# Kernel optimization log

Hardware: AMD Instinct MI355X
Metric: run time of the kernel (lower is better)

## Reference

```python
import jax, jax.numpy as jnp
import numpy as np

# Model dims (match init_kwargs)
D_MODEL = 2048
H = 16        # query heads
HKV = 4       # kv heads (GQA)
DS = 32       # semantic head dim (compressed)
DG = 32       # geometric head dim (compressed, RoPE'd)
DV = 64       # value head dim
B, T = 2, 4096
MB = 64       # mem_block
LW = 1024     # local_window
ROPE_BASE = 10000.0
NEG_INF = -1e9


def _rope(x, pos, base):
    # x: [B, h, T, d] with d even; standard rotate-half RoPE
    d = x.shape[-1]
    inv_freq = 1.0 / (base ** (jnp.arange(0, d, 2, dtype=jnp.float32) / d))
    ang = pos.astype(jnp.float32)[:, None] * inv_freq          # [T, d/2]
    cos, sin = jnp.cos(ang), jnp.sin(ang)                      # [T, d/2]
    x1, x2 = jnp.split(x, 2, axis=-1)
    return jnp.concatenate([x1 * cos - x2 * sin,
                            x2 * cos + x1 * sin], axis=-1)


def setup_inputs() -> dict:
    key = jax.random.key(0)
    ks = jax.random.split(key, 8)
    w = lambda k, sh: jax.random.normal(k, sh, jnp.float32) * 0.02
    return {
        "x": jax.random.normal(ks[0], (B, T, D_MODEL), jnp.float32),
        "Wq_sem": w(ks[1], (D_MODEL, H * DS)),
        "Wk_sem": w(ks[2], (D_MODEL, HKV * DS)),
        "Wq_geo": w(ks[3], (D_MODEL, H * DG)),
        "Wk_geo": w(ks[4], (D_MODEL, HKV * DG)),
        "Wv": w(ks[5], (D_MODEL, HKV * DV)),
        "Wo": w(ks[6], (H * DV, D_MODEL)),
        "logit_scale": jnp.zeros((H,), jnp.float32),
    }


def reference(x, Wq_sem, Wk_sem, Wq_geo, Wk_geo, Wv, Wo, logit_scale):
    Bq, Tq = x.shape[0], x.shape[1]
    split = lambda y, h, d: y.reshape(Bq, Tq, h, d).transpose(0, 2, 1, 3)
    # Decoupled projections
    q_sem = split(x @ Wq_sem, H, DS)      # [B,H,T,DS]
    k_sem = split(x @ Wk_sem, HKV, DS)    # [B,HKV,T,DS]
    q_geo = split(x @ Wq_geo, H, DG)
    k_geo = split(x @ Wk_geo, HKV, DG)
    v = split(x @ Wv, HKV, DV)            # [B,HKV,T,DV]
    pos = jnp.arange(Tq)
    # RoPE only on the geometric path
    q_geo = _rope(q_geo, pos, ROPE_BASE)
    k_geo = _rope(k_geo, pos, ROPE_BASE)
    # Memory-block summarization: mean-pool remote KV into one token per block
    remote = Tq - LW
    nblk = remote // MB
    pool = lambda a: jnp.concatenate(
        [a[:, :, :remote].reshape(Bq, HKV, nblk, MB, a.shape[-1]).mean(axis=3),
         a[:, :, remote:]], axis=2)
    k_sem2, k_geo2, v2 = pool(k_sem), pool(k_geo), pool(v)  # [B,HKV,K,*], K=nblk+LW
    k_pos = jnp.concatenate([jnp.arange(nblk) * MB + (MB - 1),
                             jnp.arange(remote, Tq)])        # [K]
    # GQA head-group broadcast
    rep = lambda a: jnp.repeat(a, H // HKV, axis=1)
    k_sem2, k_geo2, v2 = rep(k_sem2), rep(k_geo2), rep(v2)   # [B,H,K,*]
    # Decoupled scores: semantic + geometric, each with its own scale
    scores = (jnp.einsum('bhqd,bhkd->bhqk', q_sem, k_sem2) * (1.0 / jnp.sqrt(float(DS)))
              + jnp.einsum('bhqd,bhkd->bhqk', q_geo, k_geo2) * (1.0 / jnp.sqrt(float(DG))))
    # Learned per-head temperature
    scores = scores * jnp.exp(logit_scale)[None, :, None, None]
    # Causal mask over summarized key positions
    mask = k_pos[None, :] <= pos[:, None]                    # [T,K]
    scores = jnp.where(mask[None, None], scores, NEG_INF)
    probs = jax.nn.softmax(scores, axis=-1)
    out = jnp.einsum('bhqk,bhkd->bhqd', probs, v2)           # [B,H,T,DV]
    out = out.transpose(0, 2, 1, 3).reshape(Bq, Tq, H * DV)
    return out @ Wo                                          # [B,T,D_MODEL]
```

## Files before the change

### kernel.cpp

```cpp
#include <hip/hip_runtime.h>
#include <math.h>

#define B_  2
#define T_  4096
#define DM  2048
#define H_  16
#define HKV 4
#define DV_ 64
#define MB_ 64
#define LW_ 1024
#define REMOTE 3072
#define NBLK 48
#define KTOT 1072
#define NTILES 17

typedef __bf16 bf16x8 __attribute__((ext_vector_type(8)));
typedef float  f32x4  __attribute__((ext_vector_type(4)));

__device__ __forceinline__ float bf2f(unsigned short u) {
    unsigned int x = ((unsigned int)u) << 16;
    return __builtin_bit_cast(float, x);
}
__device__ __forceinline__ unsigned short f2bf(float f) {
    unsigned int x = __builtin_bit_cast(unsigned int, f);
    x = x + 0x7fffu + ((x >> 16) & 1u);
    return (unsigned short)(x >> 16);
}

__device__ __forceinline__ void gload16(const void* gsrc, unsigned short* ldst) {
    __builtin_amdgcn_global_load_lds(
        (const __attribute__((address_space(1))) void*)gsrc,
        (__attribute__((address_space(3))) void*)ldst,
        16, 0, 0);
}

__global__ void transpose_all(const float* __restrict__ Wq_sem,
                              const float* __restrict__ Wq_geo,
                              const float* __restrict__ Wk_sem,
                              const float* __restrict__ Wk_geo,
                              const float* __restrict__ Wv,
                              const float* __restrict__ Wo,
                              unsigned short* __restrict__ WcatT,
                              unsigned short* __restrict__ WoT) {
    __shared__ float tile[32][33];
    const int bid = blockIdx.x;
    const float* src; unsigned short* dst; int R, C, tiles_x, lt;
    if (bid < 1024)      { src = Wq_sem; dst = WcatT;                       R = 2048; C = 512;  tiles_x = 16; lt = bid; }
    else if (bid < 2048) { src = Wq_geo; dst = WcatT + (size_t)512  * 2048; R = 2048; C = 512;  tiles_x = 16; lt = bid - 1024; }
    else if (bid < 2304) { src = Wk_sem; dst = WcatT + (size_t)1024 * 2048; R = 2048; C = 128;  tiles_x = 4;  lt = bid - 2048; }
    else if (bid < 2560) { src = Wk_geo; dst = WcatT + (size_t)1152 * 2048; R = 2048; C = 128;  tiles_x = 4;  lt = bid - 2304; }
    else if (bid < 3072) { src = Wv;     dst = WcatT + (size_t)1280 * 2048; R = 2048; C = 256;  tiles_x = 8;  lt = bid - 2560; }
    else                 { src = Wo;     dst = WoT;                         R = 1024; C = 2048; tiles_x = 64; lt = bid - 3072; }
    const int ct = lt % tiles_x, rt = lt / tiles_x;
    const int tx = threadIdx.x, ty = threadIdx.y;
    #pragma unroll
    for (int i = ty; i < 32; i += 8)
        tile[i][tx] = src[(size_t)(rt * 32 + i) * C + ct * 32 + tx];
    __syncthreads();
    #pragma unroll
    for (int i = ty; i < 32; i += 8)
        dst[(size_t)(ct * 32 + i) * R + rt * 32 + tx] = f2bf(tile[tx][i]);
}

template<int MODE>
__global__ __launch_bounds__(256, 3) void gemmP(
    const void* __restrict__ Ap,
    const unsigned short* __restrict__ BT,
    float* __restrict__ outF,
    unsigned short* __restrict__ qcat,
    unsigned short* __restrict__ kp,
    unsigned short* __restrict__ vt,
    int M, int N, int K, int nbx)
{
    extern __shared__ __align__(16) unsigned short lds[];

    const int tid = threadIdx.x;
    const int lane = tid & 63, w = tid >> 6;
    const int wr = w >> 1, wc = w & 1;
    const int l15 = lane & 15, lg = lane >> 4;

    const int cpx = gridDim.x >> 3;
    const int swz = (blockIdx.x & 7) * cpx + (blockIdx.x >> 3);
    const int bx = swz % nbx, by = swz / nbx;
    const int row0 = by * 128, col0 = bx * 128;

    const int scol = ((lane & 3) ^ ((lane >> 3) & 3)) * 8;
    const int srA = w * 16 + (lane >> 2);
    const unsigned short* Bg = BT + (size_t)col0 * K;
    const unsigned short* Agh = (const unsigned short*)Ap + (size_t)row0 * K;

    const int ar0 = tid >> 2, ar1 = ar0 + 64, ac = tid & 3;
    const int agc0 = (ac ^ ((ar0 >> 1) & 3)) * 8;
    const int agc1 = (ac ^ ((ar1 >> 1) & 3)) * 8;
    const float* Axf = (const float*)Ap + (size_t)row0 * K;

    const int rdsw = (lg ^ ((l15 >> 1) & 3)) * 8;
    const int aoff = (wr * 64 + l15) * 32 + rdsw;
    const int boff = (wc * 64 + l15) * 32 + rdsw;

    const int NT = K >> 5;
    f32x4 acc[4][4] = {};

    auto stageB = [&](int s, int kk) {
        unsigned short* sb = lds + s * 8192 + 4096;
        #pragma unroll
        for (int j = 0; j < 2; j++)
            gload16(Bg + (size_t)(srA + j * 64) * K + kk + scol,
                    sb + (j * 256 + w * 64) * 8);
    };
    auto stageAB = [&](int s, int kk) {
        unsigned short* sa = lds + s * 8192;
        unsigned short* sb = sa + 4096;
        #pragma unroll
        for (int j = 0; j < 2; j++) {
            gload16(Agh + (size_t)(srA + j * 64) * K + kk + scol,
                    sa + (j * 256 + w * 64) * 8);
            gload16(Bg + (size_t)(srA + j * 64) * K + kk + scol,
                    sb + (j * 256 + w * 64) * 8);
        }
    };
    auto issueA = [&](float4* ra, int kk) {
        ra[0] = *(const float4*)&Axf[(size_t)ar0 * K + kk + agc0];
        ra[1] = *(const float4*)&Axf[(size_t)ar0 * K + kk + agc0 + 4];
        ra[2] = *(const float4*)&Axf[(size_t)ar1 * K + kk + agc1];
        ra[3] = *(const float4*)&Axf[(size_t)ar1 * K + kk + agc1 + 4];
    };
    auto writeA = [&](int s, const float4* ra) {
        unsigned short* sa = lds + s * 8192;
        bf16x8 v0, v1;
        v0[0] = (__bf16)ra[0].x; v0[1] = (__bf16)ra[0].y;
        v0[2] = (__bf16)ra[0].z; v0[3] = (__bf16)ra[0].w;
        v0[4] = (__bf16)ra[1].x; v0[5] = (__bf16)ra[1].y;
        v0[6] = (__bf16)ra[1].z; v0[7] = (__bf16)ra[1].w;
        v1[0] = (__bf16)ra[2].x; v1[1] = (__bf16)ra[2].y;
        v1[2] = (__bf16)ra[2].z; v1[3] = (__bf16)ra[2].w;
        v1[4] = (__bf16)ra[3].x; v1[5] = (__bf16)ra[3].y;
        v1[6] = (__bf16)ra[3].z; v1[7] = (__bf16)ra[3].w;
        *(uint4*)&sa[ar0 * 32 + ac * 8] = __builtin_bit_cast(uint4, v0);
        *(uint4*)&sa[ar1 * 32 + ac * 8] = __builtin_bit_cast(uint4, v1);
    };

    #define FRAGS_MFMA(rs_)                                                     \
        {                                                                       \
            const unsigned short* As_ = lds + (rs_) * 8192;                     \
            const unsigned short* Bs_ = As_ + 4096;                             \
            bf16x8 af[4], bfr[4];                                               \
            _Pragma("unroll")                                                   \
            for (int mf = 0; mf < 4; mf++)                                      \
                af[mf] = __builtin_bit_cast(bf16x8,                             \
                    *(const uint4*)&As_[aoff + mf * 512]);                      \
            _Pragma("unroll")                                                   \
            for (int nf = 0; nf < 4; nf++)                                      \
                bfr[nf] = __builtin_bit_cast(bf16x8,                            \
                    *(const uint4*)&Bs_[boff + nf * 512]);                      \
            __builtin_amdgcn_s_setprio(1);                                      \
            _Pragma("unroll")                                                   \
            for (int mf = 0; mf < 4; mf++)                                      \
                _Pragma("unroll")                                               \
                for (int nf = 0; nf < 4; nf++)                                  \
                    acc[mf][nf] = __builtin_amdgcn_mfma_f32_16x16x32_bf16(      \
                        af[mf], bfr[nf], acc[mf][nf], 0, 0, 0);                 \
            __builtin_amdgcn_s_setprio(0);                                      \
        }

    if (MODE == 0) {
        stageB(0, 0);
        stageB(1, 32);
        __builtin_amdgcn_sched_barrier(0);
        float4 rA[4], rB[4];
        issueA(rA, 0);
        issueA(rB, 32);
        writeA(0, rA);
        asm volatile("s_waitcnt lgkmcnt(0)" ::: "memory");
        __builtin_amdgcn_s_barrier();

        int rs = 0;
        for (int t = 0; t < NT; t += 2) {
            {
                if (t + 2 < NT) {
                    stageB(rs == 0 ? 2 : rs - 1, (t + 2) << 5);
                    __builtin_amdgcn_sched_barrier(0);
                    issueA(rA, (t + 2) << 5);
                }
                FRAGS_MFMA(rs);
                int s1 = (rs == 2) ? 0 : rs + 1;
                writeA(s1, rB);
                asm volatile("s_waitcnt vmcnt(6)" ::: "memory");
                asm volatile("s_waitcnt lgkmcnt(0)" ::: "memory");
                __builtin_amdgcn_s_barrier();
                rs = s1;
            }
            {
                if (t + 3 < NT) {
                    stageB(rs == 0 ? 2 : rs - 1, (t + 3) << 5);
                    __builtin_amdgcn_sched_barrier(0);
                    issueA(rB, (t + 3) << 5);
                }
                FRAGS_MFMA(rs);
                int s1 = (rs == 2) ? 0 : rs + 1;
                if (t + 2 < NT) writeA(s1, rA);
                asm volatile("s_waitcnt vmcnt(6)" ::: "memory");
                asm volatile("s_waitcnt lgkmcnt(0)" ::: "memory");
                __builtin_amdgcn_s_barrier();
                rs = s1;
            }
        }
    } else {
        stageAB(0, 0);
        stageAB(1, 32);
        asm volatile("s_waitcnt vmcnt(4)" ::: "memory");
        int rs = 0;
        for (int t = 0; t < NT; ++t) {
            __builtin_amdgcn_s_barrier();
            if (t + 2 < NT) stageAB(rs == 0 ? 2 : rs - 1, (t + 2) << 5);
            FRAGS_MFMA(rs);
            if (t + 2 < NT) asm volatile("s_waitcnt vmcnt(4)" ::: "memory");
            else            asm volatile("s_waitcnt vmcnt(0)" ::: "memory");
            rs = (rs == 2) ? 0 : rs + 1;
        }
    }
    #undef FRAGS_MFMA

    if (MODE == 1) {
        #pragma unroll
        for (int mf = 0; mf < 4; mf++)
            #pragma unroll
            for (int nf = 0; nf < 4; nf++)
                #pragma unroll
                for (int r = 0; r < 4; r++) {
                    int row = row0 + wr * 64 + mf * 16 + lg * 4 + r;
                    int col = col0 + wc * 64 + nf * 16 + l15;
                    outF[(size_t)row * N + col] = acc[mf][nf][r];
                }
    } else {
        const int cspan = col0 + wc * 64;
        const int tbase = row0 & 4095;
        const int bq = row0 >> 12;

        if ((cspan >= 512 && cspan < 1024) || (cspan >= 1152 && cspan < 1280)) {
            const float invf = exp2f(-(float)l15 * 0.8304820237218406f);
            #pragma unroll
            for (int mf = 0; mf < 4; mf++) {
                #pragma unroll
                for (int r = 0; r < 4; r++) {
                    float s, c;
                    sincosf((float)(tbase + wr*64 + mf*16 + lg*4 + r) * invf, &s, &c);
                    float a0 = acc[mf][0][r], a1 = acc[mf][1][r];
                    acc[mf][0][r] = a0 * c - a1 * s;
                    acc[mf][1][r] = a1 * c + a0 * s;
                    float a2 = acc[mf][2][r], a3 = acc[mf][3][r];
                    acc[mf][2][r] = a2 * c - a3 * s;
                    acc[mf][3][r] = a3 * c + a2 * s;
                }
            }
        }

        if (cspan < 1024) {
            #pragma unroll
            for (int nf = 0; nf < 4; nf++) {
                int col = cspan + nf * 16 + l15;
                int h = (col < 512) ? (col >> 5) : ((col - 512) >> 5);
                int d = (col < 512) ? (col & 31) : (32 + (col & 31));
                unsigned short* qb =
                    qcat + (((size_t)(bq * 16 + h)) * 4096 + tbase) * 64 + d;
                #pragma unroll
                for (int mf = 0; mf < 4; mf++)
                    #pragma unroll
                    for (int r = 0; r < 4; r++)
                        qb[(size_t)(wr*64 + mf*16 + lg*4 + r) * 64] =
                            f2bf(acc[mf][nf][r]);
            }
        } else if (tbase >= REMOTE) {
            #pragma unroll
            for (int nf = 0; nf < 4; nf++) {
                int col = cspan + nf * 16 + l15;
                #pragma unroll
                for (int mf = 0; mf < 4; mf++)
                    #pragma unroll
                    for (int r = 0; r < 4; r++) {
                        int key = tbase + wr*64 + mf*16 + lg*4 + r - 3024;
                        unsigned short hv = f2bf(acc[mf][nf][r]);
                        if (col < 1280) {
                            int g, dk;
                            if (col < 1152) { g = (col - 1024) >> 5; dk = col & 31; }
                            else            { g = (col - 1152) >> 5; dk = 32 + (col & 31); }
                            kp[(((size_t)(bq*4 + g)) * KTOT + key) * 64 + dk] = hv;
                        } else {
                            int g = (col - 1280) >> 6, dv = col & 63;
                            vt[(((size_t)(bq*4 + g)) * 64 + dv) * KTOT + key] = hv;
                        }
                    }
            }
        } else {
            #pragma unroll
            for (int nf = 0; nf < 4; nf++) {
                float ps = 0.f;
                #pragma unroll
                for (int mf = 0; mf < 4; mf++)
                    #pragma unroll
                    for (int r = 0; r < 4; r++) ps += acc[mf][nf][r];
                ps += __shfl_xor(ps, 16);
                ps += __shfl_xor(ps, 32);
                if (lane < 16) {
                    int col = cspan + nf * 16 + l15;
                    int key = (tbase >> 6) + wr;
                    unsigned short hv = f2bf(ps * (1.f / 64.f));
                    if (col < 1280) {
                        int g, dk;
                        if (col < 1152) { g = (col - 1024) >> 5; dk = col & 31; }
                        else            { g = (col - 1152) >> 5; dk = 32 + (col & 31); }
                        kp[(((size_t)(bq*4 + g)) * KTOT + key) * 64 + dk] = hv;
                    } else {
                        int g = (col - 1280) >> 6, dv = col & 63;
                        vt[(((size_t)(bq*4 + g)) * 64 + dv) * KTOT + key] = hv;
                    }
                }
            }
        }
    }
}

__global__ __launch_bounds__(256) void attn_fwd(
    const unsigned short* __restrict__ qcat,
    const unsigned short* __restrict__ kp,
    const unsigned short* __restrict__ vt,
    const float* __restrict__ ls,
    unsigned short* __restrict__ attn_out)
{
    __shared__ unsigned short Pl[4][32][72];

    const int tid = threadIdx.x;
    const int lane = tid & 63, w = tid >> 6;
    const int l15 = lane & 15, lg = lane >> 4;

    const int wid = blockIdx.x * 4 + w;
    const int hb = wid & 31;
    const int iu = wid >> 5;
    int i;
    if (iu < 32)       i = 127 - iu;
    else if (iu == 32) i = 0;
    else if (iu == 33) i = 1;
    else               i = iu - 32;
    const int h = hb & 15, b = hb >> 4, g = h >> 2;
    const int q0 = i * 32;

    int ktmax;
    if (q0 < 64) ktmax = NTILES;
    else {
        int lastkey = q0 + 31 - 3024;
        ktmax = (lastkey < NBLK) ? 1 : (lastkey / 64 + 1);
    }

    const float sc = __expf(ls[h]) * 0.17677669529663687f;

    bf16x8 aq[2][2];
    const unsigned short* qbase = qcat + (((size_t)(b * 16 + h)) * T_ + q0) * 64;
    #pragma unroll
    for (int rf = 0; rf < 2; rf++)
        #pragma unroll
        for (int kh = 0; kh < 2; kh++)
            aq[rf][kh] = __builtin_bit_cast(bf16x8,
                *(const uint4*)(qbase + (size_t)(rf*16 + l15)*64 + kh*32 + lg*8));

    float m[2][4], lrun[2][4];
    #pragma unroll
    for (int rf = 0; rf < 2; rf++)
        #pragma unroll
        for (int r = 0; r < 4; r++) { m[rf][r] = -1e9f; lrun[rf][r] = 0.f; }
    f32x4 oacc[2][4] = {};

    const unsigned short* kbase = kp + ((size_t)(b * 4 + g)) * KTOT * 64;
    const unsigned short* vbase = vt + ((size_t)(b * 4 + g)) * 64 * KTOT;

    for (int kt = 0; kt < ktmax; kt++) {
        const int kb = kt * 64;

        bf16x8 bk[4][2];
        #pragma unroll
        for (int nf = 0; nf < 4; nf++) {
            int krow = kb + nf*16 + l15;
            int krc = krow < KTOT ? krow : KTOT - 1;
            #pragma unroll
            for (int kh = 0; kh < 2; kh++)
                bk[nf][kh] = __builtin_bit_cast(bf16x8,
                    *(const uint4*)(kbase + (size_t)krc * 64 + kh*32 + lg*8));
        }

        f32x4 s[2][4] = {};
        #pragma unroll
        for (int rf = 0; rf < 2; rf++)
            #pragma unroll
            for (int nf = 0; nf < 4; nf++)
                #pragma unroll
                for (int kh = 0; kh < 2; kh++)
                    s[rf][nf] = __builtin_amdgcn_mfma_f32_16x16x32_bf16(
                                    aq[rf][kh], bk[nf][kh], s[rf][nf], 0, 0, 0);

        bf16x8 bv[4][2];
        #pragma unroll
        for (int nfv = 0; nfv < 4; nfv++)
            #pragma unroll
            for (int kh = 0; kh < 2; kh++) {
                int kc = kb + kh*32 + lg*8;
                int kcc = (kc + 8 <= KTOT) ? kc : KTOT - 8;
                bv[nfv][kh] = __builtin_bit_cast(bf16x8,
                    *(const uint4*)(vbase + (size_t)(nfv*16 + l15) * KTOT + kcc));
            }

        #pragma unroll
        for (int rf = 0; rf < 2; rf++) {
            #pragma unroll
            for (int r = 0; r < 4; r++) {
                const int qpos = q0 + rf*16 + lg*4 + r;
                float vals[4];
                float tmax = -INFINITY;
                #pragma unroll
                for (int nf = 0; nf < 4; nf++) {
                    int key = kb + nf*16 + l15;
                    float v = s[rf][nf][r] * sc;
                    int kpos = (key < NBLK) ? key * 64 + 63 : 3024 + key;
                    v = (key < KTOT) ? ((kpos <= qpos) ? v : -1e9f) : -INFINITY;
                    vals[nf] = v;
                    tmax = fmaxf(tmax, v);
                }
                #pragma unroll
                for (int d = 1; d < 16; d <<= 1)
                    tmax = fmaxf(tmax, __shfl_xor(tmax, d));
                float mn = fmaxf(m[rf][r], tmax);
                float scl = __expf(m[rf][r] - mn);
                m[rf][r] = mn;
                float rs = 0.f;
                #pragma unroll
                for (int nf = 0; nf < 4; nf++) {
                    unsigned short pb = f2bf(__expf(vals[nf] - mn));
                    rs += bf2f(pb);
                    Pl[w][rf*16 + lg*4 + r][nf*16 + l15] = pb;
                }
                #pragma unroll
                for (int d = 1; d < 16; d <<= 1)
                    rs += __shfl_xor(rs, d);
                lrun[rf][r] = lrun[rf][r] * scl + rs;
                #pragma unroll
                for (int nfv = 0; nfv < 4; nfv++)
                    oacc[rf][nfv][r] *= scl;
            }
        }

        #pragma unroll
        for (int rf = 0; rf < 2; rf++) {
            bf16x8 pa[2];
            #pragma unroll
            for (int kh = 0; kh < 2; kh++)
                pa[kh] = __builtin_bit_cast(bf16x8,
                    *(const uint4*)&Pl[w][rf*16 + l15][kh*32 + lg*8]);
            #pragma unroll
            for (int nfv = 0; nfv < 4; nfv++)
                #pragma unroll
                for (int kh = 0; kh < 2; kh++)
                    oacc[rf][nfv] = __builtin_amdgcn_mfma_f32_16x16x32_bf16(
                                        pa[kh], bv[nfv][kh], oacc[rf][nfv], 0, 0, 0);
        }
    }

    #pragma unroll
    for (int rf = 0; rf < 2; rf++) {
        #pragma unroll
        for (int r = 0; r < 4; r++) {
            float inv = 1.f / lrun[rf][r];
            int q = q0 + rf*16 + lg*4 + r;
            size_t obase = ((size_t)(b * T_ + q)) * 1024 + h * 64;
            #pragma unroll
            for (int nfv = 0; nfv < 4; nfv++)
                attn_out[obase + nfv*16 + l15] = f2bf(oacc[rf][nfv][r] * inv);
        }
    }
}

extern "C" void kernel_launch(void* const* d_in, const int* in_sizes, int n_in,
                              void* d_out, int out_size, void* d_ws, size_t ws_size,
                              hipStream_t stream) {
    const float* x      = (const float*)d_in[0];
    const float* Wq_sem = (const float*)d_in[1];
    const float* Wk_sem = (const float*)d_in[2];
    const float* Wq_geo = (const float*)d_in[3];
    const float* Wk_geo = (const float*)d_in[4];
    const float* Wv     = (const float*)d_in[5];
    const float* Wo     = (const float*)d_in[6];
    const float* ls     = (const float*)d_in[7];

    char* w = (char*)d_ws;
    auto alloc = [&](size_t bytes) {
        char* p = w;
        w += (bytes + 255) & ~(size_t)255;
        return p;
    };
    unsigned short* WcatT = (unsigned short*)alloc((size_t)1536 * 2048 * 2);
    unsigned short* WoT   = (unsigned short*)alloc((size_t)2048 * 1024 * 2);
    unsigned short* qcat  = (unsigned short*)alloc((size_t)2 * 16 * 4096 * 64 * 2);
    unsigned short* kp    = (unsigned short*)alloc((size_t)2 * 4 * 1072 * 64 * 2);
    unsigned short* vt    = (unsigned short*)alloc((size_t)2 * 4 * 1072 * 64 * 2);
    unsigned short* aout  = (unsigned short*)alloc((size_t)8192 * 1024 * 2);

    hipFuncSetAttribute(reinterpret_cast<const void*>(&gemmP<0>),
                        hipFuncAttributeMaxDynamicSharedMemorySize, 49152);
    hipFuncSetAttribute(reinterpret_cast<const void*>(&gemmP<1>),
                        hipFuncAttributeMaxDynamicSharedMemorySize, 49152);

    transpose_all<<<5120, dim3(32, 8), 0, stream>>>(
        Wq_sem, Wq_geo, Wk_sem, Wk_geo, Wv, Wo, WcatT, WoT);

    gemmP<0><<<768, 256, 49152, stream>>>(
        x, WcatT, nullptr, qcat, kp, vt, 8192, 1536, 2048, 12);

    attn_fwd<<<dim3(1024), 256, 0, stream>>>(qcat, kp, vt, ls, aout);

    gemmP<1><<<1024, 256, 49152, stream>>>(
        aout, WoT, (float*)d_out, nullptr, nullptr, nullptr, 8192, 2048, 1024, 16);
}
```

Before: 185.3 us.

## Split GEMM template into projection and wider-tile Wo kernels with reworked pipelining

The templated GEMM is split into two dedicated kernels. The output-projection GEMM now uses 128x256 tiles, with each wave owning a 64-column slice over all 128 rows, 72KB of LDS and half as many blocks. This raises reuse of each A/B tile per LDS load. The projection kernel's triple-buffer loop is reordered: fragments are written to LDS before the MFMA step, stage indices are computed explicitly, and the vmcnt(6) waits are dropped. Larger tiles lower occupancy (2 blocks/CU) and increase register pressure with 32 accumulators per lane. Removing the vmcnt waits could also risk a race on the async loads.

Result: faster. 179.3 us (-3.2%).

```diff
diff --git a/kernel.cpp b/kernel.cpp
--- a/kernel.cpp
+++ b/kernel.cpp
@@ -62,15 +62,13 @@
         dst[(size_t)(ct * 32 + i) * R + rt * 32 + tx] = f2bf(tile[tx][i]);
 }
 
-template<int MODE>
-__global__ __launch_bounds__(256, 3) void gemmP(
-    const void* __restrict__ Ap,
+__global__ __launch_bounds__(256, 3) void gemmProj(
+    const float* __restrict__ Axf0,
     const unsigned short* __restrict__ BT,
-    float* __restrict__ outF,
     unsigned short* __restrict__ qcat,
     unsigned short* __restrict__ kp,
     unsigned short* __restrict__ vt,
-    int M, int N, int K, int nbx)
+    int K, int nbx)
 {
     extern __shared__ __align__(16) unsigned short lds[];
 
@@ -87,12 +85,11 @@
     const int scol = ((lane & 3) ^ ((lane >> 3) & 3)) * 8;
     const int srA = w * 16 + (lane >> 2);
     const unsigned short* Bg = BT + (size_t)col0 * K;
-    const unsigned short* Agh = (const unsigned short*)Ap + (size_t)row0 * K;
 
     const int ar0 = tid >> 2, ar1 = ar0 + 64, ac = tid & 3;
     const int agc0 = (ac ^ ((ar0 >> 1) & 3)) * 8;
     const int agc1 = (ac ^ ((ar1 >> 1) & 3)) * 8;
-    const float* Axf = (const float*)Ap + (size_t)row0 * K;
+    const float* Axf = Axf0 + (size_t)row0 * K;
 
     const int rdsw = (lg ^ ((l15 >> 1) & 3)) * 8;
     const int aoff = (wr * 64 + l15) * 32 + rdsw;
@@ -107,17 +104,6 @@
         for (int j = 0; j < 2; j++)
             gload16(Bg + (size_t)(srA + j * 64) * K + kk + scol,
                     sb + (j * 256 + w * 64) * 8);
-    };
-    auto stageAB = [&](int s, int kk) {
-        unsigned short* sa = lds + s * 8192;
-        unsigned short* sb = sa + 4096;
-        #pragma unroll
-        for (int j = 0; j < 2; j++) {
-            gload16(Agh + (size_t)(srA + j * 64) * K + kk + scol,
-                    sa + (j * 256 + w * 64) * 8);
-            gload16(Bg + (size_t)(srA + j * 64) * K + kk + scol,
-                    sb + (j * 256 + w * 64) * 8);
-        }
     };
     auto issueA = [&](float4* ra, int kk) {
         ra[0] = *(const float4*)&Axf[(size_t)ar0 * K + kk + agc0];
@@ -139,172 +125,108 @@
         *(uint4*)&sa[ar0 * 32 + ac * 8] = __builtin_bit_cast(uint4, v0);
         *(uint4*)&sa[ar1 * 32 + ac * 8] = __builtin_bit_cast(uint4, v1);
     };
-
-    #define FRAGS_MFMA(rs_)                                                     \
-        {                                                                       \
-            const unsigned short* As_ = lds + (rs_) * 8192;                     \
-            const unsigned short* Bs_ = As_ + 4096;                             \
-            bf16x8 af[4], bfr[4];                                               \
-            _Pragma("unroll")                                                   \
-            for (int mf = 0; mf < 4; mf++)                                      \
-                af[mf] = __builtin_bit_cast(bf16x8,                             \
-                    *(const uint4*)&As_[aoff + mf * 512]);                      \
-            _Pragma("unroll")                                                   \
-            for (int nf = 0; nf < 4; nf++)                                      \
-                bfr[nf] = __builtin_bit_cast(bf16x8,                            \
-                    *(const uint4*)&Bs_[boff + nf * 512]);                      \
-            __builtin_amdgcn_s_setprio(1);                                      \
-            _Pragma("unroll")                                                   \
-            for (int mf = 0; mf < 4; mf++)                                      \
-                _Pragma("unroll")                                               \
-                for (int nf = 0; nf < 4; nf++)                                  \
-                    acc[mf][nf] = __builtin_amdgcn_mfma_f32_16x16x32_bf16(      \
-                        af[mf], bfr[nf], acc[mf][nf], 0, 0, 0);                 \
-            __builtin_amdgcn_s_setprio(0);                                      \
-        }
-
-    if (MODE == 0) {
-        stageB(0, 0);
-        stageB(1, 32);
-        __builtin_amdgcn_sched_barrier(0);
-        float4 rA[4], rB[4];
-        issueA(rA, 0);
-        issueA(rB, 32);
-        writeA(0, rA);
+    auto mfmaTile = [&](int rs_) {
+        const unsigned short* As_ = lds + rs_ * 8192;
+        const unsigned short* Bs_ = As_ + 4096;
+        bf16x8 af[4], bfr[4];
+        #pragma unroll
+        for (int mf = 0; mf < 4; mf++)
+            af[mf] = __builtin_bit_cast(bf16x8, *(const uint4*)&As_[aoff + mf * 512]);
+        #pragma unroll
+        for (int nf = 0; nf < 4; nf++)
+            bfr[nf] = __builtin_bit_cast(bf16x8, *(const uint4*)&Bs_[boff + nf * 512]);
+        __builtin_amdgcn_s_setprio(1);
+        #pragma unroll
+        for (int mf = 0; mf < 4; mf++)
+            #pragma unroll
+            for (int nf = 0; nf < 4; nf++)
+                acc[mf][nf] = __builtin_amdgcn_mfma_f32_16x16x32_bf16(
+                    af[mf], bfr[nf], acc[mf][nf], 0, 0, 0);
+        __builtin_amdgcn_s_setprio(0);
+    };
+
+    stageB(0, 0);
+    stageB(1, 32);
+    __builtin_amdgcn_sched_barrier(0);
+    float4 rA[4], rB[4];
+    issueA(rA, 0);
+    issueA(rB, 32);
+    writeA(0, rA);
+    asm volatile("s_waitcnt lgkmcnt(0)" ::: "memory");
+    __builtin_amdgcn_s_barrier();
+
+    int rs = 0;
+    for (int t = 0; t < NT; t += 2) {
+        const int s1 = (rs == 2) ? 0 : rs + 1;
+        const int s2 = (s1 == 2) ? 0 : s1 + 1;
+        if (t + 2 < NT) {
+            stageB(s2, (t + 2) << 5);
+            __builtin_amdgcn_sched_barrier(0);
+            issueA(rA, (t + 2) << 5);
+        }
+        writeA(s1, rB);
+        mfmaTile(rs);
         asm volatile("s_waitcnt lgkmcnt(0)" ::: "memory");
         __builtin_amdgcn_s_barrier();
-
-        int rs = 0;
-        for (int t = 0; t < NT; t += 2) {
-            {
-                if (t + 2 < NT) {
-                    stageB(rs == 0 ? 2 : rs - 1, (t + 2) << 5);
-                    __builtin_amdgcn_sched_barrier(0);
-                    issueA(rA, (t + 2) << 5);
-                }
-                FRAGS_MFMA(rs);
-                int s1 = (rs == 2) ? 0 : rs + 1;
-                writeA(s1, rB);
-                asm volatile("s_waitcnt vmcnt(6)" ::: "memory");
-                asm volatile("s_waitcnt lgkmcnt(0)" ::: "memory");
-                __builtin_amdgcn_s_barrier();
-                rs = s1;
+        if (t + 3 < NT) {
+            stageB(rs, (t + 3) << 5);
+            __builtin_amdgcn_sched_barrier(0);
+            issueA(rB, (t + 3) << 5);
+        }
+        if (t + 2 < NT) writeA(s2, rA);
+        mfmaTile(s1);
+        asm volatile("s_waitcnt lgkmcnt(0)" ::: "memory");
+        __builtin_amdgcn_s_barrier();
+        rs = s2;
+    }
+
+    const int cspan = col0 + wc * 64;
+    const int tbase = row0 & 4095;
+    const int bq = row0 >> 12;
+
+    if ((cspan >= 512 && cspan < 1024) || (cspan >= 1152 && cspan < 1280)) {
+        const float invf = exp2f(-(float)l15 * 0.8304820237218406f);
+        #pragma unroll
+        for (int mf = 0; mf < 4; mf++) {
+            #pragma unroll
+            for (int r = 0; r < 4; r++) {
+                float s, c;
+                sincosf((float)(tbase + wr*64 + mf*16 + lg*4 + r) * invf, &s, &c);
+                float a0 = acc[mf][0][r], a1 = acc[mf][1][r];
+                acc[mf][0][r] = a0 * c - a1 * s;
+                acc[mf][1][r] = a1 * c + a0 * s;
+                float a2 = acc[mf][2][r], a3 = acc[mf][3][r];
+                acc[mf][2][r] = a2 * c - a3 * s;
+                acc[mf][3][r] = a3 * c + a2 * s;
             }
-            {
-                if (t + 3 < NT) {
-                    stageB(rs == 0 ? 2 : rs - 1, (t + 3) << 5);
-                    __builtin_amdgcn_sched_barrier(0);
-                    issueA(rB, (t + 3) << 5);
-                }
-                FRAGS_MFMA(rs);
-                int s1 = (rs == 2) ? 0 : rs + 1;
-                if (t + 2 < NT) writeA(s1, rA);
-                asm volatile("s_waitcnt vmcnt(6)" ::: "memory");
-                asm volatile("s_waitcnt lgkmcnt(0)" ::: "memory");
-                __builtin_amdgcn_s_barrier();
-                rs = s1;
-            }
-        }
-    } else {
-        stageAB(0, 0);
-        stageAB(1, 32);
-        asm volatile("s_waitcnt vmcnt(4)" ::: "memory");
-        int rs = 0;
-        for (int t = 0; t < NT; ++t) {
-            __builtin_amdgcn_s_barrier();
-            if (t + 2 < NT) stageAB(rs == 0 ? 2 : rs - 1, (t + 2) << 5);
-            FRAGS_MFMA(rs);
-            if (t + 2 < NT) asm volatile("s_waitcnt vmcnt(4)" ::: "memory");
-            else            asm volatile("s_waitcnt vmcnt(0)" ::: "memory");
-            rs = (rs == 2) ? 0 : rs + 1;
-        }
-    }
-    #undef FRAGS_MFMA
-
-    if (MODE == 1) {
-        #pragma unroll
-        for (int mf = 0; mf < 4; mf++)
-            #pragma unroll
-            for (int nf = 0; nf < 4; nf++)
+        }
+    }
+
+    if (cspan < 1024) {
+        #pragma unroll
+        for (int nf = 0; nf < 4; nf++) {
+            int col = cspan + nf * 16 + l15;
+            int h = (col < 512) ? (col >> 5) : ((col - 512) >> 5);
+            int d = (col < 512) ? (col & 31) : (32 + (col & 31));
+            unsigned short* qb =
+                qcat + (((size_t)(bq * 16 + h)) * 4096 + tbase) * 64 + d;
+            #pragma unroll
+            for (int mf = 0; mf < 4; mf++)
+                #pragma unroll
+                for (int r = 0; r < 4; r++)
+                    qb[(size_t)(wr*64 + mf*16 + lg*4 + r) * 64] =
+                        f2bf(acc[mf][nf][r]);
+        }
+    } else if (tbase >= REMOTE) {
+        #pragma unroll
+        for (int nf = 0; nf < 4; nf++) {
+            int col = cspan + nf * 16 + l15;
+            #pragma unroll
+            for (int mf = 0; mf < 4; mf++)
                 #pragma unroll
                 for (int r = 0; r < 4; r++) {
-                    int row = row0 + wr * 64 + mf * 16 + lg * 4 + r;
-                    int col = col0 + wc * 64 + nf * 16 + l15;
-                    outF[(size_t)row * N + col] = acc[mf][nf][r];
-                }
-    } else {
-        const int cspan = col0 + wc * 64;
-        const int tbase = row0 & 4095;
-        const int bq = row0 >> 12;
-
-        if ((cspan >= 512 && cspan < 1024) || (cspan >= 1152 && cspan < 1280)) {
-            const float invf = exp2f(-(float)l15 * 0.8304820237218406f);
-            #pragma unroll
-            for (int mf = 0; mf < 4; mf++) {
-                #pragma unroll
-                for (int r = 0; r < 4; r++) {
-                    float s, c;
-                    sincosf((float)(tbase + wr*64 + mf*16 + lg*4 + r) * invf, &s, &c);
-                    float a0 = acc[mf][0][r], a1 = acc[mf][1][r];
-                    acc[mf][0][r] = a0 * c - a1 * s;
-                    acc[mf][1][r] = a1 * c + a0 * s;
-                    float a2 = acc[mf][2][r], a3 = acc[mf][3][r];
-                    acc[mf][2][r] = a2 * c - a3 * s;
-                    acc[mf][3][r] = a3 * c + a2 * s;
-                }
-            }
-        }
-
-        if (cspan < 1024) {
-            #pragma unroll
-            for (int nf = 0; nf < 4; nf++) {
-                int col = cspan + nf * 16 + l15;
-                int h = (col < 512) ? (col >> 5) : ((col - 512) >> 5);
-                int d = (col < 512) ? (col & 31) : (32 + (col & 31));
-                unsigned short* qb =
-                    qcat + (((size_t)(bq * 16 + h)) * 4096 + tbase) * 64 + d;
-                #pragma unroll
-                for (int mf = 0; mf < 4; mf++)
-                    #pragma unroll
-                    for (int r = 0; r < 4; r++)
-                        qb[(size_t)(wr*64 + mf*16 + lg*4 + r) * 64] =
-                            f2bf(acc[mf][nf][r]);
-            }
-        } else if (tbase >= REMOTE) {
-            #pragma unroll
-            for (int nf = 0; nf < 4; nf++) {
-                int col = cspan + nf * 16 + l15;
-                #pragma unroll
-                for (int mf = 0; mf < 4; mf++)
-                    #pragma unroll
-                    for (int r = 0; r < 4; r++) {
-                        int key = tbase + wr*64 + mf*16 + lg*4 + r - 3024;
-                        unsigned short hv = f2bf(acc[mf][nf][r]);
-                        if (col < 1280) {
-                            int g, dk;
-                            if (col < 1152) { g = (col - 1024) >> 5; dk = col & 31; }
-                            else            { g = (col - 1152) >> 5; dk = 32 + (col & 31); }
-                            kp[(((size_t)(bq*4 + g)) * KTOT + key) * 64 + dk] = hv;
-                        } else {
-                            int g = (col - 1280) >> 6, dv = col & 63;
-                            vt[(((size_t)(bq*4 + g)) * 64 + dv) * KTOT + key] = hv;
-                        }
-                    }
-            }
-        } else {
-            #pragma unroll
-            for (int nf = 0; nf < 4; nf++) {
-                float ps = 0.f;
-                #pragma unroll
-                for (int mf = 0; mf < 4; mf++)
-                    #pragma unroll
-                    for (int r = 0; r < 4; r++) ps += acc[mf][nf][r];
-                ps += __shfl_xor(ps, 16);
-                ps += __shfl_xor(ps, 32);
-                if (lane < 16) {
-                    int col = cspan + nf * 16 + l15;
-                    int key = (tbase >> 6) + wr;
-                    unsigned short hv = f2bf(ps * (1.f / 64.f));
+                    int key = tbase + wr*64 + mf*16 + lg*4 + r - 3024;
+                    unsigned short hv = f2bf(acc[mf][nf][r]);
                     if (col < 1280) {
                         int g, dk;
                         if (col < 1152) { g = (col - 1024) >> 5; dk = col & 31; }
@@ -315,9 +237,120 @@
                         vt[(((size_t)(bq*4 + g)) * 64 + dv) * KTOT + key] = hv;
                     }
                 }
+        }
+    } else {
+        #pragma unroll
+        for (int nf = 0; nf < 4; nf++) {
+            float ps = 0.f;
+            #pragma unroll
+            for (int mf = 0; mf < 4; mf++)
+                #pragma unroll
+                for (int r = 0; r < 4; r++) ps += acc[mf][nf][r];
+            ps += __shfl_xor(ps, 16);
+            ps += __shfl_xor(ps, 32);
+            if (lane < 16) {
+                int col = cspan + nf * 16 + l15;
+                int key = (tbase >> 6) + wr;
+                unsigned short hv = f2bf(ps * (1.f / 64.f));
+                if (col < 1280) {
+                    int g, dk;
+                    if (col < 1152) { g = (col - 1024) >> 5; dk = col & 31; }
+                    else            { g = (col - 1152) >> 5; dk = 32 + (col & 31); }
+                    kp[(((size_t)(bq*4 + g)) * KTOT + key) * 64 + dk] = hv;
+                } else {
+                    int g = (col - 1280) >> 6, dv = col & 63;
+                    vt[(((size_t)(bq*4 + g)) * 64 + dv) * KTOT + key] = hv;
+                }
             }
         }
     }
+}
+
+__global__ __launch_bounds__(256, 2) void gemmWo(
+    const unsigned short* __restrict__ A,
+    const unsigned short* __restrict__ BT,
+    float* __restrict__ outF,
+    int N, int K, int nbx)
+{
+    extern __shared__ __align__(16) unsigned short lds[];
+
+    const int tid = threadIdx.x;
+    const int lane = tid & 63, w = tid >> 6;
+    const int l15 = lane & 15, lg = lane >> 4;
+
+    const int cpx = gridDim.x >> 3;
+    const int swz = (blockIdx.x & 7) * cpx + (blockIdx.x >> 3);
+    const int bx = swz % nbx, by = swz / nbx;
+    const int row0 = by * 128, col0 = bx * 256;
+
+    const int scol = ((lane & 3) ^ ((lane >> 3) & 3)) * 8;
+    const int srA = w * 16 + (lane >> 2);
+    const unsigned short* Ag = A  + (size_t)row0 * K;
+    const unsigned short* Bg = BT + (size_t)col0 * K;
+
+    const int rdsw = (lg ^ ((l15 >> 1) & 3)) * 8;
+    const int aoff = l15 * 32 + rdsw;
+    const int boff = (w * 64 + l15) * 32 + rdsw;
+
+    const int NT = K >> 5;
+    f32x4 acc[8][4] = {};
+
+    auto stage = [&](int s, int kk) {
+        unsigned short* sa = lds + s * 12288;
+        unsigned short* sb = sa + 4096;
+        #pragma unroll
+        for (int j = 0; j < 2; j++)
+            gload16(Ag + (size_t)(srA + j * 64) * K + kk + scol,
+                    sa + (j * 256 + w * 64) * 8);
+        #pragma unroll
+        for (int j = 0; j < 4; j++)
+            gload16(Bg + (size_t)(srA + j * 64) * K + kk + scol,
+                    sb + (j * 256 + w * 64) * 8);
+    };
+
+    stage(0, 0);
+    stage(1, 32);
+    asm volatile("s_waitcnt vmcnt(6)" ::: "memory");
+
+    int rs = 0;
+    for (int t = 0; t < NT; ++t) {
+        __builtin_amdgcn_s_barrier();
+        if (t + 2 < NT) stage(rs == 0 ? 2 : rs - 1, (t + 2) << 5);
+
+        const unsigned short* As_ = lds + rs * 12288;
+        const unsigned short* Bs_ = As_ + 4096;
+        bf16x8 af[8], bfr[4];
+        #pragma unroll
+        for (int mf = 0; mf < 8; mf++)
+            af[mf] = __builtin_bit_cast(bf16x8, *(const uint4*)&As_[aoff + mf * 512]);
+        #pragma unroll
+        for (int nf = 0; nf < 4; nf++)
+            bfr[nf] = __builtin_bit_cast(bf16x8, *(const uint4*)&Bs_[boff + nf * 512]);
+
+        __builtin_amdgcn_s_setprio(1);
+        #pragma unroll
+        for (int mf = 0; mf < 8; mf++)
+            #pragma unroll
+            for (int nf = 0; nf < 4; nf++)
+                acc[mf][nf] = __builtin_amdgcn_mfma_f32_16x16x32_bf16(
+                                  af[mf], bfr[nf], acc[mf][nf], 0, 0, 0);
+        __builtin_amdgcn_s_setprio(0);
+
+        if (t + 2 < NT) asm volatile("s_waitcnt vmcnt(6)" ::: "memory");
+        else            asm volatile("s_waitcnt vmcnt(0)" ::: "memory");
+        rs = (rs == 2) ? 0 : rs + 1;
+    }
+
+    #pragma unroll
+    for (int mf = 0; mf < 8; mf++)
+        #pragma unroll
+        for (int nf = 0; nf < 4; nf++)
+            #pragma unroll
+            for (int r = 0; r < 4; r++) {
+                int row = row0 + mf * 16 + lg * 4 + r;
+                int col = col0 + w * 64 + nf * 16 + l15;
+                outF[(size_t)row * N + col] = acc[mf][nf][r];
+            }
 }
 
 __global__ __launch_bounds__(256) void attn_fwd(
@@ -501,19 +534,19 @@
     unsigned short* vt    = (unsigned short*)alloc((size_t)2 * 4 * 1072 * 64 * 2);
     unsigned short* aout  = (unsigned short*)alloc((size_t)8192 * 1024 * 2);
 
-    hipFuncSetAttribute(reinterpret_cast<const void*>(&gemmP<0>),
+    hipFuncSetAttribute(reinterpret_cast<const void*>(&gemmProj),
                         hipFuncAttributeMaxDynamicSharedMemorySize, 49152);
-    hipFuncSetAttribute(reinterpret_cast<const void*>(&gemmP<1>),
-                        hipFuncAttributeMaxDynamicSharedMemorySize, 49152);
+    hipFuncSetAttribute(reinterpret_cast<const void*>(&gemmWo),
+                        hipFuncAttributeMaxDynamicSharedMemorySize, 73728);
 
     transpose_all<<<5120, dim3(32, 8), 0, stream>>>(
         Wq_sem, Wq_geo, Wk_sem, Wk_geo, Wv, Wo, WcatT, WoT);
 
-    gemmP<0><<<768, 256, 49152, stream>>>(
-        x, WcatT, nullptr, qcat, kp, vt, 8192, 1536, 2048, 12);
+    gemmProj<<<768, 256, 49152, stream>>>(
+        x, WcatT, qcat, kp, vt, 2048, 12);
 
     attn_fwd<<<dim3(1024), 256, 0, stream>>>(qcat, kp, vt, ls, aout);
 
-    gemmP<1><<<1024, 256, 49152, stream>>>(
-        aout, WoT, (float*)d_out, nullptr, nullptr, nullptr, 8192, 2048, 1024, 16);
-}
+    gemmWo<<<512, 256, 73728, stream>>>(
+        aout, WoT, (float*)d_out, 2048, 1024, 8);
+}
```
